# Kernel optimization log

Measured on AMD Instinct MI355X. Metric: run time of the kernel, lower is better.

## Reference

```python
import jax, jax.numpy as jnp
import numpy as np

KH, KW = 7, 7      # t2t kernel_size
ST = 3             # stride
PD = 3             # padding
K = KH * KW        # 49 taps per patch


def _patch_indices(H, W):
    """Linear indices into the padded (Hp,Wp) image for every (patch l, tap k)."""
    Hp, Wp = H + 2 * PD, W + 2 * PD
    oh = (H + 2 * PD - KH) // ST + 1
    ow = (W + 2 * PD - KW) // ST + 1
    ki, kj = np.meshgrid(np.arange(KH), np.arange(KW), indexing='ij')
    rows = (np.arange(oh) * ST)[:, None, None, None] + ki[None, None]   # (oh,1,kh,kw)
    cols = (np.arange(ow) * ST)[None, :, None, None] + kj[None, None]   # (1,ow,kh,kw)
    idx = (rows * Wp + cols).reshape(oh * ow, K)                        # (L, 49)
    return jnp.asarray(idx), Hp, Wp, oh * ow


def setup_inputs() -> dict:
    key = jax.random.key(0)
    k1, k2, k3 = jax.random.split(key, 3)
    b, n, d, hd = 2, 5760, 512, 1960
    return {
        'x': jax.random.normal(k1, (b, n, d), dtype=jnp.float32),
        'W1': jax.random.normal(k2, (d, hd), dtype=jnp.float32) * 0.02,
        'b1': jnp.zeros((hd,), dtype=jnp.float32),
        'W2': jax.random.normal(k3, (hd, d), dtype=jnp.float32) * 0.02,
        'b2': jnp.zeros((d,), dtype=jnp.float32),
        'out_h': 60,
        'out_w': 108,
    }


def reference(x, W1, b1, W2, b2, out_h, out_w):
    H, W = int(out_h), int(out_w)
    idx, Hp, Wp, L = _patch_indices(H, W)          # idx: (L, 49)
    idxf = idx.reshape(-1)                         # (L*49,)

    b, n, _ = x.shape
    h = x @ W1 + b1                                # (b, n, 1960)
    hd = h.shape[-1]
    C = hd // K                                    # 40 fold channels
    Bp = (b * n) // L                              # fold batch (= b * t)

    # fold input layout: (Bp, C, K, L) -> scatter-add into padded image
    patches = h.reshape(Bp, L, C, K)
    vals = jnp.transpose(patches, (0, 2, 1, 3)).reshape(Bp * C, L * K)
    img = jnp.zeros((Bp * C, Hp * Wp), x.dtype).at[:, idxf].add(vals)

    # overlap-count normalizer (fold of ones), same for every batch/channel
    count = jnp.zeros((Hp * Wp,), x.dtype).at[idxf].add(jnp.ones_like(idxf, x.dtype))

    # crop padding (as F.fold does), normalize, re-pad with zeros (as F.unfold does)
    img = img.reshape(Bp, C, Hp, Wp)[:, :, PD:PD + H, PD:PD + W]
    cnt = count.reshape(Hp, Wp)[PD:PD + H, PD:PD + W]
    img = img / cnt
    flat = jnp.pad(img, ((0, 0), (0, 0), (PD, PD), (PD, PD))).reshape(Bp * C, Hp * Wp)

    # unfold: gather the same taps back, restore (b, n, hd) token layout
    g = flat[:, idxf].reshape(Bp, C, L, K)
    g = jnp.transpose(g, (0, 2, 1, 3)).reshape(b, n, hd)

    return jax.nn.gelu(g, approximate=False) @ W2 + b2
```

## Files before the change

kernel.cpp:

```cpp
#include <hip/hip_runtime.h>

typedef _Float16 f16;
typedef __attribute__((ext_vector_type(8))) _Float16 half8;
typedef __attribute__((ext_vector_type(4))) _Float16 half4;
typedef __attribute__((ext_vector_type(4))) float f32x4;

#define LDS_AS __attribute__((address_space(3)))
#define GLB_AS __attribute__((address_space(1)))

__device__ __forceinline__ void load16_lds(const f16* g, f16* l) {
    __builtin_amdgcn_global_load_lds((GLB_AS void*)(g), (LDS_AS void*)(l), 16, 0, 0);
}

#define WAIT8_BARRIER()  asm volatile("s_waitcnt vmcnt(8)\n\ts_barrier" ::: "memory")
#define WAIT4_BARRIER()  asm volatile("s_waitcnt vmcnt(4)\n\ts_barrier" ::: "memory")
#define WAIT0_BARRIER()  asm volatile("s_waitcnt vmcnt(0)\n\ts_barrier" ::: "memory")
#define ENDBAR()         asm volatile("s_waitcnt lgkmcnt(0)\n\ts_barrier" ::: "memory")

__global__ __launch_bounds__(256, 3) void gemm1(
    const f16* __restrict__ A, const f16* __restrict__ Bt,
    const float* __restrict__ bias, f16* __restrict__ C)
{
    const int id  = blockIdx.x;
    const int xcd = id & 7;
    const int r   = id >> 3;
    const int mt  = r & 15;
    const int nt  = xcd + 8 * (r >> 4);
    if (nt >= 90) return;
    const int m0 = mt * 128, n0 = nt * 128;
    const int K = 512, ldc = 11520;

    __shared__ f16 smem[24576];
    const int tid  = threadIdx.x;
    const int wave = tid >> 6;
    const int lane = tid & 63;

    const int s1 = tid + 256;
    const f16* gA0 = A  + (m0 + (tid >> 2)) * K + (tid & 3) * 8;
    const f16* gA1 = A  + (m0 + (s1 >> 2)) * K + (s1 & 3) * 8;
    const f16* gB0 = Bt + (n0 + (tid >> 2)) * K + (tid & 3) * 8;
    const f16* gB1 = Bt + (n0 + (s1 >> 2)) * K + (s1 & 3) * 8;

    const int wm = (wave >> 1) * 64;
    const int wn = (wave & 1) * 64;
    const int lr = lane & 15;
    const int k8 = (lane >> 4) * 8;

    f32x4 acc[4][4];
#pragma unroll
    for (int i = 0; i < 4; ++i)
#pragma unroll
        for (int j = 0; j < 4; ++j) acc[i][j] = f32x4{0.f, 0.f, 0.f, 0.f};

#define G1_ISSUE(st, k0) do { \
    f16* sb_ = &smem[(st) * 8192]; \
    load16_lds(gA0 + (k0), sb_ + wave * 512); \
    load16_lds(gA1 + (k0), sb_ + 2048 + wave * 512); \
    load16_lds(gB0 + (k0), sb_ + 4096 + wave * 512); \
    load16_lds(gB1 + (k0), sb_ + 6144 + wave * 512); \
} while (0)

    G1_ISSUE(0, 0);
    G1_ISSUE(1, 32);
    const int NS = 16;
    int cur = 0;
    for (int s = 0; s < NS; ++s) {
        if (s + 2 < NS) {
            int pre = cur + 2; if (pre >= 3) pre -= 3;
            G1_ISSUE(pre, (s + 2) * 32);
        }
        const int rem = NS - 1 - s;
        if (rem >= 2)      WAIT8_BARRIER();
        else if (rem == 1) WAIT4_BARRIER();
        else               WAIT0_BARRIER();
        const f16* sa = &smem[cur * 8192];
        half8 af[4], bf[4];
#pragma unroll
        for (int i = 0; i < 4; ++i)
            af[i] = *(const half8*)&sa[(wm + i * 16 + lr) * 32 + k8];
#pragma unroll
        for (int j = 0; j < 4; ++j)
            bf[j] = *(const half8*)&sa[4096 + (wn + j * 16 + lr) * 32 + k8];
#pragma unroll
        for (int i = 0; i < 4; ++i)
#pragma unroll
            for (int j = 0; j < 4; ++j)
                acc[i][j] = __builtin_amdgcn_mfma_f32_16x16x32_f16(
                    af[i], bf[j], acc[i][j], 0, 0, 0);
        ENDBAR();
        ++cur; if (cur >= 3) cur = 0;
    }

#pragma unroll
    for (int i = 0; i < 4; ++i) {
#pragma unroll
        for (int rr = 0; rr < 4; ++rr) {
            const int row = m0 + wm + i * 16 + (lane >> 4) * 4 + rr;
            const float bvr = (row < 1960) ? bias[row] : 0.f;
#pragma unroll
            for (int j = 0; j < 4; ++j) {
                const int col = n0 + wn + j * 16 + lr;
                C[row * ldc + col] = (f16)(acc[i][j][rr] + bvr);
            }
        }
    }
}

__global__ __launch_bounds__(256, 2) void gemm2(
    const f16* __restrict__ A, const f16* __restrict__ Bt,
    const float* __restrict__ bias, float* __restrict__ Cout)
{
    const int id  = blockIdx.x;
    const int xcd = id & 7;
    const int j2  = id >> 3;
    const int nt  = j2 & 3;
    const int mt  = (j2 >> 2) * 8 + xcd;
    if (mt >= 90) return;
    const int m0 = mt * 128, n0 = nt * 128;

    __shared__ f16 smem[24576];
    const int tid  = threadIdx.x;
    const int wave = tid >> 6;
    const int lane = tid & 63;

    const int s1 = tid + 256;
    const f16* gA0 = A  + (m0 + (tid >> 2)) * 2048 + (tid & 3) * 8;
    const f16* gA1 = A  + (m0 + (s1 >> 2)) * 2048 + (s1 & 3) * 8;
    const f16* gB0 = Bt + (n0 + (tid >> 2)) * 2048 + (tid & 3) * 8;
    const f16* gB1 = Bt + (n0 + (s1 >> 2)) * 2048 + (s1 & 3) * 8;

    const int wm = (wave >> 1) * 64;
    const int wn = (wave & 1) * 64;
    const int lr = lane & 15;
    const int k8 = (lane >> 4) * 8;

    f32x4 acc[4][4];
#pragma unroll
    for (int i = 0; i < 4; ++i)
#pragma unroll
        for (int j = 0; j < 4; ++j) acc[i][j] = f32x4{0.f, 0.f, 0.f, 0.f};

#define G2_ISSUE(st, k0) do { \
    f16* sb_ = &smem[(st) * 8192]; \
    load16_lds(gA0 + (k0), sb_ + wave * 512); \
    load16_lds(gA1 + (k0), sb_ + 2048 + wave * 512); \
    load16_lds(gB0 + (k0), sb_ + 4096 + wave * 512); \
    load16_lds(gB1 + (k0), sb_ + 6144 + wave * 512); \
} while (0)

    G2_ISSUE(0, 0);
    G2_ISSUE(1, 32);
    const int NS = 64;
    int cur = 0;
    for (int s = 0; s < NS; ++s) {
        if (s + 2 < NS) {
            int pre = cur + 2; if (pre >= 3) pre -= 3;
            G2_ISSUE(pre, (s + 2) * 32);
        }
        const int rem = NS - 1 - s;
        if (rem >= 2)      WAIT8_BARRIER();
        else if (rem == 1) WAIT4_BARRIER();
        else               WAIT0_BARRIER();
        const f16* sa = &smem[cur * 8192];
        half8 af[4], bf[4];
#pragma unroll
        for (int i = 0; i < 4; ++i)
            af[i] = *(const half8*)&sa[(wm + i * 16 + lr) * 32 + k8];
#pragma unroll
        for (int j = 0; j < 4; ++j)
            bf[j] = *(const half8*)&sa[4096 + (wn + j * 16 + lr) * 32 + k8];
#pragma unroll
        for (int i = 0; i < 4; ++i)
#pragma unroll
            for (int j = 0; j < 4; ++j)
                acc[i][j] = __builtin_amdgcn_mfma_f32_16x16x32_f16(
                    af[i], bf[j], acc[i][j], 0, 0, 0);
        ENDBAR();
        ++cur; if (cur >= 3) cur = 0;
    }

#pragma unroll
    for (int j = 0; j < 4; ++j) {
        const int col = n0 + wn + j * 16 + lr;
        const float bv = bias[col];
#pragma unroll
        for (int i = 0; i < 4; ++i) {
            const int rbase = m0 + wm + i * 16 + (lane >> 4) * 4;
#pragma unroll
            for (int rr = 0; rr < 4; ++rr)
                Cout[(rbase + rr) * 512 + col] = acc[i][j][rr] + bv;
        }
    }
}

__global__ __launch_bounds__(512) void fold_unfold(
    const f16* __restrict__ h_t, f16* __restrict__ g16)
{
    __shared__ f16 stg[21168];
    __shared__ f16 ch[3876];
    const int bx = blockIdx.x;
    const int bc = bx >> 1, h = bx & 1;
    const int bp = bc / 40, cch = bc % 40;
    const int tid = threadIdx.x;
    const int ohlo = h * 8;
    const int rowbase = h * 30;

    {
        const f16* src0 = h_t + cch * 49 * 11520 + bp * 720 + ohlo * 36;
        for (int s = tid; s < 2646; s += 512) {
            const int n = s / 54, i = s - n * 54;
            load16_lds(src0 + n * 11520 + i * 8, &stg[s * 8]);
        }
    }
    WAIT0_BARRIER();

    {
        const int c  = tid & 127;
        const int rl = tid >> 7;
        int kjs[3], ows[3], nc = 0;
        int qc = 0, cm = 0;
        if (c < 114) {
            qc = c / 3; cm = c - 3 * qc;
#pragma unroll
            for (int t = 0; t < 3; ++t) {
                const int kj = cm + 3 * t, ow = qc - t;
                if (kj < 7 && ow >= 0 && ow < 36) { kjs[nc] = kj; ows[nc] = ow; ++nc; }
            }
        }
#pragma unroll
        for (int p = 0; p < 9; ++p) {
            const int rloc = rl + 4 * p;
            if (rloc >= 34) break;
            const int r = rowbase + rloc;
            float outv = 0.f;
            if (c >= 3 && c < 111 && r >= 3 && r < 63) {
                const int qr = r / 3, rm = r % 3;
                float sum = 0.f;
                int cnt = 0;
#pragma unroll
                for (int t = 0; t < 3; ++t) {
                    const int ki = rm + 3 * t, oh = qr - t;
                    if (ki < 7 && oh >= 0 && oh < 20) {
                        const int rowoff = (oh - ohlo) * 36;
                        for (int b = 0; b < nc; ++b)
                            sum += (float)stg[(ki * 7 + kjs[b]) * 432 + rowoff + ows[b]];
                        cnt += nc;
                    }
                }
                const float xv = sum / (float)cnt;
                const float arg = xv * (0.7978845608028654f
                                        + 0.035677408136300125f * xv * xv);
                const float e = __expf(2.f * arg);
                outv = 0.5f * xv * (2.f - 2.f / (e + 1.f));
            }
            if (c < 114) ch[rloc * 114 + c] = (f16)outv;
        }
    }
    ENDBAR();

    if (tid < 490) {
        const int k  = tid % 49;
        const int l0 = tid / 49;
        const int ki = k / 7, kj = k - ki * 7;
        int pix = ki * 114 + l0 * 3 + kj;
        int ow  = l0;
        f16* gdst = g16 + (bp * 720 + h * 360 + l0) * 2048 + cch * 49 + k;
#pragma unroll 4
        for (int step = 0; step < 36; ++step) {
            *gdst = ch[pix];
            gdst += 10 * 2048;
            ow += 10;
            if (ow >= 36) { ow -= 36; pix += 264; }
            else          { pix += 30; }
        }
    }
    if (cch >= 36) {
        const int cb = 1960 + (cch - 36) * 22;
        for (int flat = tid; flat < 360 * 22; flat += 512) {
            const int l = h * 360 + flat / 22, k = flat - (flat / 22) * 22;
            g16[(bp * 720 + l) * 2048 + cb + k] = (f16)0.f;
        }
    }
}

__global__ __launch_bounds__(256) void prep(
    const float* __restrict__ x, f16* __restrict__ xh,
    const float* __restrict__ W1, f16* __restrict__ W1t,
    const float* __restrict__ W2, f16* __restrict__ W2t)
{
    __shared__ float tile[32][33];
    const int b = blockIdx.x, t = threadIdx.x;
    if (b < 5760) {
        const int i = b * 256 + t;
        const float4 v = ((const float4*)x)[i];
        half4 o;
        o[0] = (f16)v.x; o[1] = (f16)v.y; o[2] = (f16)v.z; o[3] = (f16)v.w;
        ((half4*)xh)[i] = o;
        return;
    }
    const float* src; f16* dst; int R, C, Rp, Cp, bx, by;
    if (b < 6784) {
        const int local = b - 5760;
        bx = local & 15; by = local >> 4;
        src = W1; dst = W1t; R = 512; C = 1960; Rp = 512; Cp = 2048;
    } else {
        const int local = b - 6784;
        bx = local & 63; by = local >> 6;
        src = W2; dst = W2t; R = 1960; C = 512; Rp = 2048; Cp = 512;
    }
    const int r0 = bx * 32, c0 = by * 32;
    const int tx = t & 31, ty = t >> 5;
#pragma unroll
    for (int i = 0; i < 32; i += 8) {
        const int r = r0 + ty + i, c = c0 + tx;
        tile[ty + i][tx] = (r < R && c < C) ? src[r * C + c] : 0.f;
    }
    __syncthreads();
#pragma unroll
    for (int i = 0; i < 32; i += 8) {
        const int c = c0 + ty + i, r = r0 + tx;
        if (c < Cp && r < Rp) dst[c * Rp + r] = (f16)tile[tx][ty + i];
    }
}

extern "C" void kernel_launch(void* const* d_in, const int* in_sizes, int n_in,
                              void* d_out, int out_size, void* d_ws, size_t ws_size,
                              hipStream_t stream)
{
    const float* x  = (const float*)d_in[0];
    const float* W1 = (const float*)d_in[1];
    const float* b1 = (const float*)d_in[2];
    const float* W2 = (const float*)d_in[3];
    const float* b2 = (const float*)d_in[4];

    char* ws = (char*)d_ws;
    f16* xh   = (f16*)(ws);
    f16* W1t  = (f16*)(ws + 11796480);
    f16* W2t  = (f16*)(ws + 11796480 + 2097152);
    f16* h_t  = (f16*)(ws + 11796480 + 2 * 2097152);
    f16* g16  = (f16*)(ws + 11796480 + 2 * 2097152 + 47185920);

    prep<<<dim3(7808), dim3(256), 0, stream>>>(x, xh, W1, W1t, W2, W2t);
    gemm1<<<dim3(1536), dim3(256), 0, stream>>>(W1t, xh, b1, h_t);
    fold_unfold<<<dim3(1280), dim3(512), 0, stream>>>(h_t, g16);
    gemm2<<<dim3(384), dim3(256), 0, stream>>>(g16, W2t, b2, (float*)d_out);
}
```

Measured before the change: 195.7 us.

## Use BK=64 double-buffered K pipeline in gemm2 instead of BK=32 triple buffer

gemm2's K loop changes from 64 steps of 32 with three LDS stages to 32 steps of 64 with two stages. Each stage now loads 128x64 tiles of A and B, eight 16-byte loads per thread, and the compute unrolls two 32-wide k-substeps. This halves the number of barriers and loop iterations and issues larger transfers per step. The cost is a shallower prefetch (one stage ahead instead of two), more LDS (64KB), and a 64-half row stride that may cause LDS bank conflicts on the half8 reads.

```diff
diff --git a/kernel.cpp b/kernel.cpp
--- a/kernel.cpp
+++ b/kernel.cpp
@@ -118,16 +118,13 @@
     if (mt >= 90) return;
     const int m0 = mt * 128, n0 = nt * 128;
 
-    __shared__ f16 smem[24576];
+    __shared__ f16 smem[32768];
     const int tid  = threadIdx.x;
     const int wave = tid >> 6;
     const int lane = tid & 63;
 
-    const int s1 = tid + 256;
-    const f16* gA0 = A  + (m0 + (tid >> 2)) * 2048 + (tid & 3) * 8;
-    const f16* gA1 = A  + (m0 + (s1 >> 2)) * 2048 + (s1 & 3) * 8;
-    const f16* gB0 = Bt + (n0 + (tid >> 2)) * 2048 + (tid & 3) * 8;
-    const f16* gB1 = Bt + (n0 + (s1 >> 2)) * 2048 + (s1 & 3) * 8;
+    const f16* gA = A  + (m0 + (tid >> 3)) * 2048 + (tid & 7) * 8;
+    const f16* gB = Bt + (n0 + (tid >> 3)) * 2048 + (tid & 7) * 8;
 
     const int wm = (wave >> 1) * 64;
     const int wn = (wave & 1) * 64;
@@ -141,42 +138,47 @@
         for (int j = 0; j < 4; ++j) acc[i][j] = f32x4{0.f, 0.f, 0.f, 0.f};
 
 #define G2_ISSUE(st, k0) do { \
-    f16* sb_ = &smem[(st) * 8192]; \
-    load16_lds(gA0 + (k0), sb_ + wave * 512); \
-    load16_lds(gA1 + (k0), sb_ + 2048 + wave * 512); \
-    load16_lds(gB0 + (k0), sb_ + 4096 + wave * 512); \
-    load16_lds(gB1 + (k0), sb_ + 6144 + wave * 512); \
+    f16* as_ = &smem[(st) * 16384]; \
+    f16* bs_ = as_ + 8192; \
+    load16_lds(gA + (k0),              as_ + tid * 8); \
+    load16_lds(gA + 32 * 2048 + (k0),  as_ + 2048 + tid * 8); \
+    load16_lds(gA + 64 * 2048 + (k0),  as_ + 4096 + tid * 8); \
+    load16_lds(gA + 96 * 2048 + (k0),  as_ + 6144 + tid * 8); \
+    load16_lds(gB + (k0),              bs_ + tid * 8); \
+    load16_lds(gB + 32 * 2048 + (k0),  bs_ + 2048 + tid * 8); \
+    load16_lds(gB + 64 * 2048 + (k0),  bs_ + 4096 + tid * 8); \
+    load16_lds(gB + 96 * 2048 + (k0),  bs_ + 6144 + tid * 8); \
 } while (0)
 
     G2_ISSUE(0, 0);
-    G2_ISSUE(1, 32);
-    const int NS = 64;
-    int cur = 0;
+    const int NS = 32;
     for (int s = 0; s < NS; ++s) {
-        if (s + 2 < NS) {
-            int pre = cur + 2; if (pre >= 3) pre -= 3;
-            G2_ISSUE(pre, (s + 2) * 32);
-        }
-        const int rem = NS - 1 - s;
-        if (rem >= 2)      WAIT8_BARRIER();
-        else if (rem == 1) WAIT4_BARRIER();
-        else               WAIT0_BARRIER();
-        const f16* sa = &smem[cur * 8192];
-        half8 af[4], bf[4];
-#pragma unroll
-        for (int i = 0; i < 4; ++i)
-            af[i] = *(const half8*)&sa[(wm + i * 16 + lr) * 32 + k8];
-#pragma unroll
-        for (int j = 0; j < 4; ++j)
-            bf[j] = *(const half8*)&sa[4096 + (wn + j * 16 + lr) * 32 + k8];
-#pragma unroll
-        for (int i = 0; i < 4; ++i)
+        const int cur = s & 1;
+        if (s + 1 < NS) {
+            G2_ISSUE(cur ^ 1, (s + 1) * 64);
+            WAIT8_BARRIER();
+        } else {
+            WAIT0_BARRIER();
+        }
+        const f16* sa = &smem[cur * 16384];
+        const f16* sb = sa + 8192;
+#pragma unroll
+        for (int ks = 0; ks < 2; ++ks) {
+            half8 af[4], bf[4];
+#pragma unroll
+            for (int i = 0; i < 4; ++i)
+                af[i] = *(const half8*)&sa[(wm + i * 16 + lr) * 64 + ks * 32 + k8];
 #pragma unroll
             for (int j = 0; j < 4; ++j)
-                acc[i][j] = __builtin_amdgcn_mfma_f32_16x16x32_f16(
-                    af[i], bf[j], acc[i][j], 0, 0, 0);
+                bf[j] = *(const half8*)&sb[(wn + j * 16 + lr) * 64 + ks * 32 + k8];
+#pragma unroll
+            for (int i = 0; i < 4; ++i)
+#pragma unroll
+                for (int j = 0; j < 4; ++j)
+                    acc[i][j] = __builtin_amdgcn_mfma_f32_16x16x32_f16(
+                        af[i], bf[j], acc[i][j], 0, 0, 0);
+        }
         ENDBAR();
-        ++cur; if (cur >= 3) cur = 0;
     }
 
 #pragma unroll
```

After: 199.4 us. About the same (+1.9%).
